# Performance work log

Hardware: AMD Instinct MI355X
Metric: run time of the kernel (lower is better)

Reference implementation:

```python
import jax, jax.numpy as jnp
import numpy as np

B, SQ, SK, D = 8, 2048, 2048, 128


def setup_inputs() -> dict:
    key = jax.random.key(0)
    kq, kk, kv = jax.random.split(key, 3)
    Q = jax.random.normal(kq, (B, SQ, D), dtype=jnp.float32)
    K = jax.random.normal(kk, (B, SK, D), dtype=jnp.float32)
    V = jax.random.normal(kv, (B, SK, D), dtype=jnp.float32)
    return {"Q": Q, "K": K, "V": V}


def reference(Q, K, V):
    d_k = K.shape[2]  # NOTE: module divides by d_k, not sqrt(d_k)
    # scores: [B, Sq, Sk]
    scores = jnp.einsum('bqd,bkd->bqk', Q, K) / d_k
    # unconventional softmax over the batch dim (dim=0), as in the source
    attn = jax.nn.softmax(scores, axis=0)
    # output: [B, Sq, D]
    return jnp.einsum('bqk,bkd->bqd', attn, V)
```

## Files before the change

### kernel.cpp

```cpp
#include <hip/hip_runtime.h>
#include <hip/hip_bf16.h>

#define B_   8
#define SQ_  2048
#define SK_  2048
#define D_   128

typedef __attribute__((ext_vector_type(8))) _Float16 f16x8;
typedef __attribute__((ext_vector_type(4))) _Float16 f16x4;
typedef __attribute__((ext_vector_type(4))) float    f32x4;

#define QK_BSTRIDE (128 * 4 * 64 * 8)
#define VF_BSTRIDE (64 * 8 * 64 * 8)

__device__ __forceinline__ void dma16(const void* g, void* l) {
    __builtin_amdgcn_global_load_lds(
        (const __attribute__((address_space(1))) unsigned int*)g,
        (__attribute__((address_space(3))) unsigned int*)l, 16, 0, 0);
}

__global__ __launch_bounds__(256)
void prep(const float* __restrict__ Q, const float* __restrict__ K,
          const float* __restrict__ V,
          _Float16* __restrict__ Qf, _Float16* __restrict__ Kf,
          _Float16* __restrict__ Vf) {
    __shared__ _Float16 T[64][136];
    const int bid = blockIdx.x;
    if (bid < 2048) {
        const float* src = (bid >= 1024) ? K : Q;
        _Float16*    dst = (bid >= 1024) ? Kf : Qf;
        int gid = (bid & 1023) * 256 + threadIdx.x;
        int l  = gid & 63;
        int ks = (gid >> 6) & 3;
        int t  = (gid >> 8) & 127;
        int b  = gid >> 15;
        const float* p = src + ((size_t)b * 2048 + t * 16 + (l & 15)) * 128
                             + ks * 32 + (l >> 4) * 8;
        f32x4 a = *(const f32x4*)p;
        f32x4 c = *(const f32x4*)(p + 4);
        f16x8 r;
        r[0] = (_Float16)a[0]; r[1] = (_Float16)a[1];
        r[2] = (_Float16)a[2]; r[3] = (_Float16)a[3];
        r[4] = (_Float16)c[0]; r[5] = (_Float16)c[1];
        r[6] = (_Float16)c[2]; r[7] = (_Float16)c[3];
        *(f16x8*)(dst + (size_t)gid * 8) = r;
    } else {
        const int vb = bid - 2048;
        const int b  = vb >> 5;
        const int kb = vb & 31;
        const int t  = threadIdx.x;
        const int row = t >> 2, c0 = (t & 3) * 32;
        const float* src = V + ((size_t)b * SK_ + kb * 64 + row) * D_ + c0;
#pragma unroll
        for (int u = 0; u < 8; ++u) {
            f32x4 v = *(const f32x4*)(src + u * 4);
            f16x4 h;
            h[0] = (_Float16)v[0]; h[1] = (_Float16)v[1];
            h[2] = (_Float16)v[2]; h[3] = (_Float16)v[3];
            *(f16x4*)&T[row][c0 + u * 4] = h;
        }
        __syncthreads();
#pragma unroll
        for (int u = 0; u < 4; ++u) {
            int s   = u * 256 + t;
            int l   = s & 63;
            int dt  = (s >> 6) & 7;
            int ktl = s >> 9;
            int hi  = l >> 4, ql = l & 15;
            f16x8 r;
#pragma unroll
            for (int j = 0; j < 8; ++j) r[j] = T[ktl * 32 + hi * 8 + j][dt * 16 + ql];
            *(f16x8*)(Vf + (((size_t)b * 64 + kb * 2 + ktl) * 8 + dt) * 512 + (size_t)l * 8) = r;
        }
    }
}

__global__ __launch_bounds__(512, 4)
void zred(const _Float16* __restrict__ Qf, const _Float16* __restrict__ Kf,
          _Float16* __restrict__ Pf, int nqt, int qoff16) {
    __shared__ __attribute__((aligned(16))) _Float16 E[8][64][64];
    const int bid   = blockIdx.x;
    const int qtile = bid >> 5;
    const int ktile = bid & 31;
    const int b  = threadIdx.x >> 6;
    const int l  = threadIdx.x & 63;
    const int hi = l >> 4, ql = l & 15;

    const _Float16* Qb = Qf + (size_t)b * QK_BSTRIDE;
    const _Float16* Kb = Kf + (size_t)b * QK_BSTRIDE;

    f32x4 s[4][4] = {};
#pragma unroll
    for (int ks = 0; ks < 4; ++ks) {
        f16x8 kf[4];
#pragma unroll
        for (int kk = 0; kk < 4; ++kk)
            kf[kk] = *(const f16x8*)(Kb + ((((size_t)ktile * 4 + kk) * 4 + ks) * 64 + l) * 8);
#pragma unroll
        for (int qq = 0; qq < 4; ++qq) {
            f16x8 qv = *(const f16x8*)(Qb + ((((size_t)(qoff16 + qtile * 4 + qq)) * 4 + ks) * 64 + l) * 8);
#pragma unroll
            for (int kk = 0; kk < 4; ++kk)
                s[kk][qq] = __builtin_amdgcn_mfma_f32_16x16x32_f16(kf[kk], qv, s[kk][qq], 0, 0, 0);
        }
    }

    f16x4* E4 = (f16x4*)&E[0][0][0];
#pragma unroll
    for (int kk = 0; kk < 4; ++kk)
#pragma unroll
        for (int qq = 0; qq < 4; ++qq) {
            f16x4 e;
#pragma unroll
            for (int r = 0; r < 4; ++r)
                e[r] = (_Float16)__expf(s[kk][qq][r] * 0.0078125f);
            int q = qq * 16 + ql;
            int k = kk * 16 + hi * 4;
            int g16 = ((b * 64 + q) << 3) + ((k >> 3) ^ (q & 7));
            E4[g16 * 2 + ((k >> 2) & 1)] = e;
        }
    __syncthreads();

    const int t    = threadIdx.x;
    const int ktl  = t >> 8;
    const int qq2  = (t >> 6) & 3;
    const int l2   = t & 63;
    const int hi2  = l2 >> 4, ql2 = l2 & 15;
    const int q_loc  = qq2 * 16 + ql2;
    const int k0_loc = ktl * 32 + hi2 * 8;
    const f16x8* E8  = (const f16x8*)&E[0][0][0];
    const int eidx   = (q_loc << 3) + ((k0_loc >> 3) ^ (q_loc & 7));

    f16x8 z = E8[eidx];
#pragma unroll
    for (int bb = 1; bb < 8; ++bb) z = z + E8[bb * 512 + eidx];
    float inv[8];
#pragma unroll
    for (int j = 0; j < 8; ++j) inv[j] = __builtin_amdgcn_rcpf((float)z[j]);

    const size_t pbase = (((size_t)(qtile * 4 + qq2)) * 64 + (ktile * 2 + ktl)) * 512 + (size_t)l2 * 8;
#pragma unroll
    for (int bb = 0; bb < 8; ++bb) {
        f16x8 e = E8[bb * 512 + eidx];
        f16x8 p;
#pragma unroll
        for (int j = 0; j < 8; ++j) p[j] = (_Float16)((float)e[j] * inv[j]);
        *(f16x8*)(Pf + (size_t)bb * nqt * 32768 + pbase) = p;
    }
}

__global__ __launch_bounds__(512)
void av(const _Float16* __restrict__ Pf, const _Float16* __restrict__ Vf,
        float* __restrict__ out, int nqt, int qoff) {
    __shared__ __attribute__((aligned(16))) _Float16 lds[3 * 12288];

    const int bid = blockIdx.x;
    const int b   = bid & 7;
    const int mt  = bid >> 3;
    const int w   = threadIdx.x >> 6;
    const int l   = threadIdx.x & 63;
    const int wq  = w >> 2;
    const int wd  = w & 3;
    const int hi  = l >> 4, ql = l & 15;

    const _Float16* Pb = Pf + (size_t)b * nqt * 32768;
    const _Float16* Vb = Vf + (size_t)b * VF_BSTRIDE;

#define STAGE(bufi, kt2) do {                                                  \
    _Float16* dst0 = (_Float16*)lds + (size_t)(bufi) * 12288;                  \
    _Pragma("unroll")                                                          \
    for (int u = 0; u < 3; ++u) {                                              \
        int c = w * 3 + u;                                                     \
        const _Float16* srcp;                                                  \
        if (c < 8)                                                             \
            srcp = Pb + (((size_t)(mt * 4 + (c >> 1))) * 64 + ((kt2) * 2 + (c & 1))) * 512 + (size_t)l * 8; \
        else {                                                                 \
            int cv = c - 8;                                                    \
            srcp = Vb + (((size_t)((kt2) * 2 + (cv >> 3))) * 8 + (cv & 7)) * 512 + (size_t)l * 8; \
        }                                                                      \
        dma16(srcp, dst0 + c * 512);                                           \
    }                                                                          \
} while (0)

#define MFMA_PHASE(bufi) do {                                                  \
    const _Float16* Bf = (const _Float16*)lds + (size_t)(bufi) * 12288;        \
    _Pragma("unroll")                                                          \
    for (int ktl = 0; ktl < 2; ++ktl) {                                        \
        f16x8 pfr[2], vfr[2];                                                  \
        _Pragma("unroll")                                                      \
        for (int i = 0; i < 2; ++i)                                            \
            pfr[i] = *(const f16x8*)(Bf + ((wq * 2 + i) * 2 + ktl) * 512 + l * 8); \
        _Pragma("unroll")                                                      \
        for (int j = 0; j < 2; ++j)                                            \
            vfr[j] = *(const f16x8*)(Bf + 4096 + (ktl * 8 + wd * 2 + j) * 512 + l * 8); \
        _Pragma("unroll")                                                      \
        for (int i = 0; i < 2; ++i)                                            \
            _Pragma("unroll")                                                  \
            for (int j = 0; j < 2; ++j)                                        \
                acc[i][j] = __builtin_amdgcn_mfma_f32_16x16x32_f16(pfr[i], vfr[j], acc[i][j], 0, 0, 0); \
    }                                                                          \
} while (0)

    f32x4 acc[2][2] = {};
    STAGE(0, 0);
    STAGE(1, 1);
    for (int kt2 = 0; kt2 < 32; ++kt2) {
        if (kt2 < 30) {
            STAGE((kt2 + 2) % 3, kt2 + 2);
            asm volatile("s_waitcnt vmcnt(6)" ::: "memory");
        } else if (kt2 == 30) {
            asm volatile("s_waitcnt vmcnt(3)" ::: "memory");
        } else {
            asm volatile("s_waitcnt vmcnt(0)" ::: "memory");
        }
        __builtin_amdgcn_s_barrier();
        __builtin_amdgcn_sched_barrier(0);
        MFMA_PHASE(kt2 % 3);
        __builtin_amdgcn_s_barrier();
    }

    const int q0 = qoff + mt * 64 + wq * 32;
#pragma unroll
    for (int i = 0; i < 2; ++i)
#pragma unroll
        for (int j = 0; j < 2; ++j)
#pragma unroll
            for (int r = 0; r < 4; ++r)
                out[((size_t)b * SQ_ + q0 + i * 16 + hi * 4 + r) * D_ + (wd * 2 + j) * 16 + ql]
                    = acc[i][j][r];
#undef STAGE
#undef MFMA_PHASE
}

extern "C" void kernel_launch(void* const* d_in, const int* in_sizes, int n_in,
                              void* d_out, int out_size, void* d_ws, size_t ws_size,
                              hipStream_t stream) {
    const float* Q = (const float*)d_in[0];
    const float* K = (const float*)d_in[1];
    const float* V = (const float*)d_in[2];
    float* out = (float*)d_out;

    _Float16* Qf = (_Float16*)d_ws;
    _Float16* Kf = Qf + (size_t)B_ * QK_BSTRIDE;
    _Float16* Vf = Kf + (size_t)B_ * QK_BSTRIDE;
    _Float16* Pf = Vf + (size_t)B_ * VF_BSTRIDE;

    size_t used  = (size_t)(12 * 1024 * 1024);
    size_t avail = ws_size > used ? (ws_size - used) / 2 : 0;
    int nq = 2048;
    while (nq > 64 && (size_t)nq * 16384 > avail) nq >>= 1;
    int nchunks = 2048 / nq;
    int nqt = nq / 16;

    prep<<<2048 + 256, 256, 0, stream>>>(Q, K, V, Qf, Kf, Vf);

    for (int ci = 0; ci < nchunks; ++ci) {
        int qoff = ci * nq;
        zred<<<(nq / 64) * 32, 512, 0, stream>>>(Qf, Kf, Pf, nqt, qoff >> 4);
        av<<<(nq / 64) * 8, 512, 0, stream>>>(Pf, Vf, out, nqt, qoff);
    }
}
```

Baseline: 58.26 us.

## Store only reciprocal batch sums and recompute QK^T exp inside fused AV kernel

zred now writes only the per-(q,k) reciprocal of the batch-summed exponentials (one fp16 plane) instead of the full 8-batch normalized P tensor. A new fused kernel recomputes Q·K^T and exp per batch, multiplies by the stored reciprocal and feeds the product straight into the P·V MFMAs. It also splits the key dimension across waves and reduces the two partial outputs through LDS. This removes the large P write/read traffic and the chunking loop, at the cost of doing the QK^T matmul and exp twice and using a larger LDS footprint per block.

```diff
diff --git a/kernel.cpp b/kernel.cpp
--- a/kernel.cpp
+++ b/kernel.cpp
@@ -77,7 +77,7 @@
 
 __global__ __launch_bounds__(512, 4)
 void zred(const _Float16* __restrict__ Qf, const _Float16* __restrict__ Kf,
-          _Float16* __restrict__ Pf, int nqt, int qoff16) {
+          _Float16* __restrict__ RZ) {
     __shared__ __attribute__((aligned(16))) _Float16 E[8][64][64];
     const int bid   = blockIdx.x;
     const int qtile = bid >> 5;
@@ -98,7 +98,7 @@
             kf[kk] = *(const f16x8*)(Kb + ((((size_t)ktile * 4 + kk) * 4 + ks) * 64 + l) * 8);
 #pragma unroll
         for (int qq = 0; qq < 4; ++qq) {
-            f16x8 qv = *(const f16x8*)(Qb + ((((size_t)(qoff16 + qtile * 4 + qq)) * 4 + ks) * 64 + l) * 8);
+            f16x8 qv = *(const f16x8*)(Qb + ((((size_t)qtile * 4 + qq) * 4 + ks) * 64 + l) * 8);
 #pragma unroll
             for (int kk = 0; kk < 4; ++kk)
                 s[kk][qq] = __builtin_amdgcn_mfma_f32_16x16x32_f16(kf[kk], qv, s[kk][qq], 0, 0, 0);
@@ -134,102 +134,143 @@
     f16x8 z = E8[eidx];
 #pragma unroll
     for (int bb = 1; bb < 8; ++bb) z = z + E8[bb * 512 + eidx];
-    float inv[8];
-#pragma unroll
-    for (int j = 0; j < 8; ++j) inv[j] = __builtin_amdgcn_rcpf((float)z[j]);
-
-    const size_t pbase = (((size_t)(qtile * 4 + qq2)) * 64 + (ktile * 2 + ktl)) * 512 + (size_t)l2 * 8;
-#pragma unroll
-    for (int bb = 0; bb < 8; ++bb) {
-        f16x8 e = E8[bb * 512 + eidx];
-        f16x8 p;
-#pragma unroll
-        for (int j = 0; j < 8; ++j) p[j] = (_Float16)((float)e[j] * inv[j]);
-        *(f16x8*)(Pf + (size_t)bb * nqt * 32768 + pbase) = p;
-    }
+
+    f16x8 rz8;
+#pragma unroll
+    for (int j = 0; j < 8; ++j)
+        rz8[j] = (_Float16)__builtin_amdgcn_rcpf((float)z[j]);
+
+    *(f16x8*)(RZ + (((size_t)(qtile * 4 + qq2)) * 64 + (ktile * 2 + ktl)) * 512
+                 + (size_t)l2 * 8) = rz8;
 }
 
 __global__ __launch_bounds__(512)
-void av(const _Float16* __restrict__ Pf, const _Float16* __restrict__ Vf,
-        float* __restrict__ out, int nqt, int qoff) {
-    __shared__ __attribute__((aligned(16))) _Float16 lds[3 * 12288];
+void fav(const _Float16* __restrict__ Qf, const _Float16* __restrict__ Kf,
+         const _Float16* __restrict__ Vf, const _Float16* __restrict__ RZ,
+         float* __restrict__ out) {
+    __shared__ __attribute__((aligned(16))) _Float16 lds[3 * 20480 + 2 * 4096];
 
     const int bid = blockIdx.x;
     const int b   = bid & 7;
     const int mt  = bid >> 3;
     const int w   = threadIdx.x >> 6;
     const int l   = threadIdx.x & 63;
-    const int wq  = w >> 2;
-    const int wd  = w & 3;
     const int hi  = l >> 4, ql = l & 15;
-
-    const _Float16* Pb = Pf + (size_t)b * nqt * 32768;
+    const int kkq = w >> 1, qqp = w & 1;
+    const int pqqp = w >> 2, pdth = (w >> 1) & 1, pktl = w & 1;
+
+    const _Float16* Qb = Qf + (size_t)b * QK_BSTRIDE;
+    const _Float16* Kb = Kf + (size_t)b * QK_BSTRIDE;
     const _Float16* Vb = Vf + (size_t)b * VF_BSTRIDE;
 
-#define STAGE(bufi, kt2) do {                                                  \
-    _Float16* dst0 = (_Float16*)lds + (size_t)(bufi) * 12288;                  \
+    f16x8 qf[2][4];
+#pragma unroll
+    for (int i = 0; i < 2; ++i)
+#pragma unroll
+        for (int ks = 0; ks < 4; ++ks)
+            qf[i][ks] = *(const f16x8*)(Qb + ((((size_t)(mt * 4 + qqp * 2 + i)) * 4 + ks) * 64 + l) * 8);
+
+#define STAGE(bufi, it2) do {                                                  \
+    _Float16* dst0 = (_Float16*)lds + (size_t)(bufi) * 20480;                  \
     _Pragma("unroll")                                                          \
-    for (int u = 0; u < 3; ++u) {                                              \
-        int c = w * 3 + u;                                                     \
+    for (int u = 0; u < 5; ++u) {                                              \
+        int c = w * 5 + u;                                                     \
         const _Float16* srcp;                                                  \
-        if (c < 8)                                                             \
-            srcp = Pb + (((size_t)(mt * 4 + (c >> 1))) * 64 + ((kt2) * 2 + (c & 1))) * 512 + (size_t)l * 8; \
-        else {                                                                 \
-            int cv = c - 8;                                                    \
-            srcp = Vb + (((size_t)((kt2) * 2 + (cv >> 3))) * 8 + (cv & 7)) * 512 + (size_t)l * 8; \
+        if (c < 16)                                                            \
+            srcp = Kb + (((size_t)((it2) * 4 + (c >> 2))) * 4 + (c & 3)) * 512 + (size_t)l * 8; \
+        else if (c < 32) {                                                     \
+            int cv = c - 16;                                                   \
+            srcp = Vb + (((size_t)((it2) * 2 + (cv >> 3))) * 8 + (cv & 7)) * 512 + (size_t)l * 8; \
+        } else {                                                               \
+            int cr = c - 32;                                                   \
+            srcp = RZ + (((size_t)(mt * 4 + (cr >> 1))) * 64 + ((it2) * 2 + (cr & 1))) * 512 + (size_t)l * 8; \
         }                                                                      \
         dma16(srcp, dst0 + c * 512);                                           \
     }                                                                          \
 } while (0)
 
-#define MFMA_PHASE(bufi) do {                                                  \
-    const _Float16* Bf = (const _Float16*)lds + (size_t)(bufi) * 12288;        \
-    _Pragma("unroll")                                                          \
-    for (int ktl = 0; ktl < 2; ++ktl) {                                        \
-        f16x8 pfr[2], vfr[2];                                                  \
-        _Pragma("unroll")                                                      \
-        for (int i = 0; i < 2; ++i)                                            \
-            pfr[i] = *(const f16x8*)(Bf + ((wq * 2 + i) * 2 + ktl) * 512 + l * 8); \
-        _Pragma("unroll")                                                      \
-        for (int j = 0; j < 2; ++j)                                            \
-            vfr[j] = *(const f16x8*)(Bf + 4096 + (ktl * 8 + wd * 2 + j) * 512 + l * 8); \
-        _Pragma("unroll")                                                      \
-        for (int i = 0; i < 2; ++i)                                            \
-            _Pragma("unroll")                                                  \
-            for (int j = 0; j < 2; ++j)                                        \
-                acc[i][j] = __builtin_amdgcn_mfma_f32_16x16x32_f16(pfr[i], vfr[j], acc[i][j], 0, 0, 0); \
-    }                                                                          \
-} while (0)
-
-    f32x4 acc[2][2] = {};
+    f32x4 acc[2][4] = {};
     STAGE(0, 0);
     STAGE(1, 1);
-    for (int kt2 = 0; kt2 < 32; ++kt2) {
-        if (kt2 < 30) {
-            STAGE((kt2 + 2) % 3, kt2 + 2);
-            asm volatile("s_waitcnt vmcnt(6)" ::: "memory");
-        } else if (kt2 == 30) {
-            asm volatile("s_waitcnt vmcnt(3)" ::: "memory");
-        } else {
-            asm volatile("s_waitcnt vmcnt(0)" ::: "memory");
-        }
+
+    for (int it = 0; it < 32; ++it) {
+        if (it < 31) asm volatile("s_waitcnt vmcnt(5)" ::: "memory");
+        else         asm volatile("s_waitcnt vmcnt(0)" ::: "memory");
         __builtin_amdgcn_s_barrier();
         __builtin_amdgcn_sched_barrier(0);
-        MFMA_PHASE(kt2 % 3);
+        if (it < 30) STAGE((it + 2) % 3, it + 2);
+        const _Float16* SB = (const _Float16*)lds + (size_t)(it % 3) * 20480;
+
+        f32x4 s0 = {}, s1 = {};
+#pragma unroll
+        for (int ks = 0; ks < 4; ++ks) {
+            f16x8 kf8 = *(const f16x8*)(SB + (kkq * 4 + ks) * 512 + l * 8);
+            s0 = __builtin_amdgcn_mfma_f32_16x16x32_f16(kf8, qf[0][ks], s0, 0, 0, 0);
+            s1 = __builtin_amdgcn_mfma_f32_16x16x32_f16(kf8, qf[1][ks], s1, 0, 0, 0);
+        }
+
+        _Float16* Ebuf = (_Float16*)lds + 61440 + (it & 1) * 4096;
+        f16x4* E4 = (f16x4*)Ebuf;
+        {
+            const int k_loc = kkq * 16 + hi * 4;
+            f16x4 e0, e1;
+#pragma unroll
+            for (int r = 0; r < 4; ++r) {
+                e0[r] = (_Float16)__expf(s0[r] * 0.0078125f);
+                e1[r] = (_Float16)__expf(s1[r] * 0.0078125f);
+            }
+            int q0 = (qqp * 2 + 0) * 16 + ql;
+            int q1 = (qqp * 2 + 1) * 16 + ql;
+            E4[(((q0 << 3) + ((k_loc >> 3) ^ (q0 & 7))) << 1) + ((k_loc >> 2) & 1)] = e0;
+            E4[(((q1 << 3) + ((k_loc >> 3) ^ (q1 & 7))) << 1) + ((k_loc >> 2) & 1)] = e1;
+        }
+        asm volatile("s_waitcnt lgkmcnt(0)" ::: "memory");
         __builtin_amdgcn_s_barrier();
-    }
-
-    const int q0 = qoff + mt * 64 + wq * 32;
-#pragma unroll
-    for (int i = 0; i < 2; ++i)
-#pragma unroll
-        for (int j = 0; j < 2; ++j)
-#pragma unroll
-            for (int r = 0; r < 4; ++r)
-                out[((size_t)b * SQ_ + q0 + i * 16 + hi * 4 + r) * D_ + (wd * 2 + j) * 16 + ql]
-                    = acc[i][j][r];
+        __builtin_amdgcn_sched_barrier(0);
+
+        const f16x8* E8 = (const f16x8*)Ebuf;
+        f16x8 p8[2];
+#pragma unroll
+        for (int i = 0; i < 2; ++i) {
+            int q_loc = (pqqp * 2 + i) * 16 + ql;
+            int k0    = pktl * 32 + hi * 8;
+            f16x8 e8  = E8[(q_loc << 3) + ((k0 >> 3) ^ (q_loc & 7))];
+            f16x8 rz8 = *(const f16x8*)(SB + (32 + (pqqp * 2 + i) * 2 + pktl) * 512 + l * 8);
+            p8[i] = e8 * rz8;
+        }
+#pragma unroll
+        for (int j = 0; j < 4; ++j) {
+            f16x8 v8 = *(const f16x8*)(SB + (16 + pktl * 8 + pdth * 4 + j) * 512 + l * 8);
+            acc[0][j] = __builtin_amdgcn_mfma_f32_16x16x32_f16(p8[0], v8, acc[0][j], 0, 0, 0);
+            acc[1][j] = __builtin_amdgcn_mfma_f32_16x16x32_f16(p8[1], v8, acc[1][j], 0, 0, 0);
+        }
+    }
 #undef STAGE
-#undef MFMA_PHASE
+
+    __syncthreads();
+    float* OB = (float*)lds;
+    if (pktl == 1) {
+#pragma unroll
+        for (int i = 0; i < 2; ++i)
+#pragma unroll
+            for (int j = 0; j < 4; ++j)
+                *(f32x4*)(OB + (size_t)(((pqqp * 2 + i) * 8) + pdth * 4 + j) * 256 + l * 4)
+                    = acc[i][j];
+    }
+    __syncthreads();
+    if (pktl == 0) {
+#pragma unroll
+        for (int i = 0; i < 2; ++i)
+#pragma unroll
+            for (int j = 0; j < 4; ++j) {
+                f32x4 o = acc[i][j]
+                        + *(const f32x4*)(OB + (size_t)(((pqqp * 2 + i) * 8) + pdth * 4 + j) * 256 + l * 4);
+#pragma unroll
+                for (int r = 0; r < 4; ++r)
+                    out[((size_t)b * SQ_ + mt * 64 + (pqqp * 2 + i) * 16 + hi * 4 + r) * D_
+                        + (pdth * 4 + j) * 16 + ql] = o[r];
+            }
+    }
 }
 
 extern "C" void kernel_launch(void* const* d_in, const int* in_sizes, int n_in,
@@ -243,20 +284,9 @@
     _Float16* Qf = (_Float16*)d_ws;
     _Float16* Kf = Qf + (size_t)B_ * QK_BSTRIDE;
     _Float16* Vf = Kf + (size_t)B_ * QK_BSTRIDE;
-    _Float16* Pf = Vf + (size_t)B_ * VF_BSTRIDE;
-
-    size_t used  = (size_t)(12 * 1024 * 1024);
-    size_t avail = ws_size > used ? (ws_size - used) / 2 : 0;
-    int nq = 2048;
-    while (nq > 64 && (size_t)nq * 16384 > avail) nq >>= 1;
-    int nchunks = 2048 / nq;
-    int nqt = nq / 16;
+    _Float16* RZ = Vf + (size_t)B_ * VF_BSTRIDE;
 
     prep<<<2048 + 256, 256, 0, stream>>>(Q, K, V, Qf, Kf, Vf);
-
-    for (int ci = 0; ci < nchunks; ++ci) {
-        int qoff = ci * nq;
-        zred<<<(nq / 64) * 32, 512, 0, stream>>>(Qf, Kf, Pf, nqt, qoff >> 4);
-        av<<<(nq / 64) * 8, 512, 0, stream>>>(Pf, Vf, out, nqt, qoff);
-    }
-}
+    zred<<<1024, 512, 0, stream>>>(Qf, Kf, RZ);
+    fav<<<256, 512, 0, stream>>>(Qf, Kf, Vf, RZ, out);
+}
```

New measurement: 66.62 us. 1.14x slower.
